# Optimization experiments

Hardware: AMD Instinct MI355X
Metric: run time of the kernel (lower is better)

Reference implementation:

```python
import jax, jax.numpy as jnp
import numpy as np

B, T, D_IN, H, D_OUT = 64, 512, 512, 1024, 512

def _uniform(key, shape, bound):
    return jax.random.uniform(key, shape, jnp.float32, -bound, bound)

def setup_inputs() -> dict:
    key = jax.random.key(0)
    ks = jax.random.split(key, 12)
    bnd = 1.0 / np.sqrt(H)  # PyTorch nn.RNN / nn.Linear init bound
    return {
        "x": jax.random.normal(ks[0], (B, T, D_IN), jnp.float32),
        "W_ih0": _uniform(ks[1], (H, D_IN), bnd),
        "W_hh0": _uniform(ks[2], (H, H), bnd),
        "b_ih0": _uniform(ks[3], (H,), bnd),
        "b_hh0": _uniform(ks[4], (H,), bnd),
        "W_ih1": _uniform(ks[5], (H, H), bnd),
        "W_hh1": _uniform(ks[6], (H, H), bnd),
        "b_ih1": _uniform(ks[7], (H,), bnd),
        "b_hh1": _uniform(ks[8], (H,), bnd),
        "W_fc": _uniform(ks[9], (D_OUT, H), bnd),
        "b_fc": _uniform(ks[10], (D_OUT,), bnd),
    }

def _rnn_layer(seq, W_ih, W_hh, b_ih, b_hh):
    # seq: [B, T, D]; tanh vanilla RNN, h0 = 0 (as in the torch forward)
    pre = jnp.einsum('btd,hd->bth', seq, W_ih) + b_ih  # input GEMM batched over time
    h0 = jnp.zeros((seq.shape[0], W_hh.shape[0]), seq.dtype)
    def step(h, p):
        h = jnp.tanh(p + h @ W_hh.T + b_hh)
        return h, h
    _, hs = jax.lax.scan(step, h0, jnp.swapaxes(pre, 0, 1))  # [T, B, H]
    return jnp.swapaxes(hs, 0, 1)  # [B, T, H]

def reference(x, W_ih0, W_hh0, b_ih0, b_hh0, W_ih1, W_hh1, b_ih1, b_hh1, W_fc, b_fc):
    h1 = _rnn_layer(x, W_ih0, W_hh0, b_ih0, b_hh0)
    h2 = _rnn_layer(h1, W_ih1, W_hh1, b_ih1, b_hh1)
    last = h2[:, -1, :]  # only the final timestep feeds the head
    return last @ W_fc.T + b_fc
```

## Files before the change

### kernel.cpp

```cpp
#include <hip/hip_runtime.h>
#include <stdint.h>

#define BB   64
#define TT   512
#define DIN  512
#define HH   1024
#define DOUT 512

#define GROUPS        4
#define ROWS          16
#define WGS_PER_GROUP 16
#define NSLICE        64
#define THREADS       512
#define NW            8
#define PSTR          18
#define PBUF          (NW * 4 * 16 * PSTR)
#define SENT          0x7fff7fffu

typedef __attribute__((ext_vector_type(8))) short frag8;
typedef __attribute__((ext_vector_type(4))) float f32x4;
typedef __attribute__((ext_vector_type(4))) unsigned int u32x4;

union U4F8 { u32x4 u; frag8 f; };

__device__ __forceinline__ float bf2f(unsigned short u) {
  union { unsigned int i; float f; } v; v.i = ((unsigned int)u) << 16; return v.f;
}
__device__ __forceinline__ unsigned short f2bf(float f) {
  union { float f; unsigned int i; } v; v.f = f;
  unsigned int x = v.i;
  x += 0x7fffu + ((x >> 16) & 1u);
  return (unsigned short)(x >> 16);
}
__device__ __forceinline__ frag8 ld8f32(const float* p) {
  frag8 r;
#pragma unroll
  for (int j = 0; j < 8; ++j) r[j] = (short)f2bf(p[j]);
  return r;
}

__device__ __forceinline__ bool ldx4_poll(frag8 a[4], const unsigned short* p) {
  u32x4 t0, t1, t2, t3;
  asm volatile(
      "global_load_dwordx4 %0, %4, off sc1\n\t"
      "global_load_dwordx4 %1, %4, off offset:64 sc1\n\t"
      "global_load_dwordx4 %2, %4, off offset:128 sc1\n\t"
      "global_load_dwordx4 %3, %4, off offset:192 sc1\n\t"
      "s_waitcnt vmcnt(0)"
      : "=&v"(t0), "=&v"(t1), "=&v"(t2), "=&v"(t3)
      : "v"(p)
      : "memory");
  bool ok = (t0[0] != SENT) & (t0[1] != SENT) & (t0[2] != SENT) & (t0[3] != SENT)
          & (t1[0] != SENT) & (t1[1] != SENT) & (t1[2] != SENT) & (t1[3] != SENT)
          & (t2[0] != SENT) & (t2[1] != SENT) & (t2[2] != SENT) & (t2[3] != SENT)
          & (t3[0] != SENT) & (t3[1] != SENT) & (t3[2] != SENT) & (t3[3] != SENT);
  U4F8 u;
  u.u = t0; a[0] = u.f;  u.u = t1; a[1] = u.f;
  u.u = t2; a[2] = u.f;  u.u = t3; a[3] = u.f;
  return __ballot(ok) == ~0ull;
}
__device__ __forceinline__ void st32_sc1(unsigned int* p, unsigned int v) {
  asm volatile("global_store_dword %0, %1, off sc1" :: "v"(p), "v"(v) : "memory");
}

template<int KIN, bool L0>
__device__ void scan_body(const void* Xv,
                          const float* Wih, const float* Whh,
                          const float* bih, const float* bhh,
                          unsigned short* S,
                          int g, int s, float* parts)
{
  constexpr int KIT_IN = KIN / (NW * 32);
  constexpr int KIT_HH = HH  / (NW * 32);

  const int j0  = s * NSLICE;
  const int r0  = g * ROWS;
  const int tid = threadIdx.x;
  const int w   = tid >> 6;
  const int l   = tid & 63;
  const int lm  = l & 15;
  const int lq  = l >> 4;

  frag8 wih_f[KIT_IN][4];
  frag8 whh_f[KIT_HH][4];
#pragma unroll
  for (int kit = 0; kit < KIT_IN; ++kit)
#pragma unroll
    for (int nt = 0; nt < 4; ++nt) {
      int n = j0 + nt * 16 + lm;
      int k = w * (KIN / NW) + kit * 32 + lq * 8;
      wih_f[kit][nt] = ld8f32(Wih + (size_t)n * KIN + k);
    }
#pragma unroll
  for (int kit = 0; kit < KIT_HH; ++kit)
#pragma unroll
    for (int nt = 0; nt < 4; ++nt) {
      int n = j0 + nt * 16 + lm;
      int k = w * (HH / NW) + kit * 32 + lq * 8;
      whh_f[kit][nt] = ld8f32(Whh + (size_t)n * HH + k);
    }

  const int erow = tid & 15;
  const int ecg  = tid >> 4;
  float bias2[2];
#pragma unroll
  for (int j = 0; j < 2; ++j) {
    int c = j0 + ecg * 2 + j;
    bias2[j] = bih[c] + bhh[c];
  }

  const size_t koff = (size_t)w * (KIN / NW) + (size_t)lq * 8;

  float4 xa[2 * KIT_IN];
  frag8  xf[KIT_IN];
  if constexpr (L0) {
    const float* xr = (const float*)Xv + ((size_t)(r0 + lm) * TT + 0) * KIN + koff;
#pragma unroll
    for (int kit = 0; kit < KIT_IN; ++kit) {
      xa[2 * kit]     = *(const float4*)(xr + kit * 32);
      xa[2 * kit + 1] = *(const float4*)(xr + kit * 32 + 4);
    }
  } else {
    const unsigned short* px = (const unsigned short*)Xv
        + ((size_t)(r0 + lm) * TT + 0) * KIN + koff;
    while (!ldx4_poll(xf, px)) {}
  }

  for (int t = 0; t < TT; ++t) {
    f32x4 acc[4];
#pragma unroll
    for (int nt = 0; nt < 4; ++nt) acc[nt] = (f32x4){0.f, 0.f, 0.f, 0.f};

    if constexpr (L0) {
#pragma unroll
      for (int kit = 0; kit < KIT_IN; ++kit) {
        const float* f0 = (const float*)&xa[2 * kit];
        const float* f1 = (const float*)&xa[2 * kit + 1];
        frag8 a;
#pragma unroll
        for (int j = 0; j < 4; ++j) {
          a[j]     = (short)f2bf(f0[j]);
          a[4 + j] = (short)f2bf(f1[j]);
        }
#pragma unroll
        for (int nt = 0; nt < 4; ++nt)
          acc[nt] = __builtin_amdgcn_mfma_f32_16x16x32_bf16(a, wih_f[kit][nt], acc[nt], 0, 0, 0);
      }
    } else {
#pragma unroll
      for (int kit = 0; kit < KIT_IN; ++kit)
#pragma unroll
        for (int nt = 0; nt < 4; ++nt)
          acc[nt] = __builtin_amdgcn_mfma_f32_16x16x32_bf16(xf[kit], wih_f[kit][nt], acc[nt], 0, 0, 0);
    }

    if (t > 0) {
      const unsigned short* ph = S + ((size_t)(r0 + lm) * TT + (t - 1)) * HH
                                   + (size_t)w * (HH / NW) + lq * 8;
      frag8 hf[KIT_HH];
      while (!ldx4_poll(hf, ph)) {}
      if constexpr (L0) {
        if (t + 1 < TT) {
          const float* xr = (const float*)Xv
              + ((size_t)(r0 + lm) * TT + (t + 1)) * KIN + koff;
#pragma unroll
          for (int kit = 0; kit < KIT_IN; ++kit) {
            xa[2 * kit]     = *(const float4*)(xr + kit * 32);
            xa[2 * kit + 1] = *(const float4*)(xr + kit * 32 + 4);
          }
        }
      }
#pragma unroll
      for (int kit = 0; kit < KIT_HH; ++kit)
#pragma unroll
        for (int nt = 0; nt < 4; ++nt)
          acc[nt] = __builtin_amdgcn_mfma_f32_16x16x32_bf16(hf[kit], whh_f[kit][nt], acc[nt], 0, 0, 0);
    } else if constexpr (L0) {
      const float* xr = (const float*)Xv + ((size_t)(r0 + lm) * TT + 1) * KIN + koff;
#pragma unroll
      for (int kit = 0; kit < KIT_IN; ++kit) {
        xa[2 * kit]     = *(const float4*)(xr + kit * 32);
        xa[2 * kit + 1] = *(const float4*)(xr + kit * 32 + 4);
      }
    }

    float* pb = parts + (t & 1) * PBUF;
#pragma unroll
    for (int nt = 0; nt < 4; ++nt)
#pragma unroll
      for (int r = 0; r < 4; ++r)
        pb[((w * 4 + nt) * 16 + lq * 4 + r) * PSTR + lm] = acc[nt][r];
    __syncthreads();

    unsigned int hb2 = 0;
#pragma unroll
    for (int j = 0; j < 2; ++j) {
      int c  = ecg * 2 + j;
      int nt = c >> 4;
      int lc = c & 15;
      float sm = 0.f;
#pragma unroll
      for (int w8 = 0; w8 < NW; ++w8)
        sm += pb[((w8 * 4 + nt) * 16 + erow) * PSTR + lc];
      float u = sm + bias2[j];
      float e = __expf(2.0f * u);
      float hv = 1.0f - 2.0f / (e + 1.0f);
      hb2 |= (unsigned int)f2bf(hv) << (16 * j);
    }
    unsigned short* dst = S + ((size_t)(r0 + erow) * TT + t) * HH + j0 + ecg * 2;
    st32_sc1((unsigned int*)dst, hb2);

    if constexpr (!L0) {
      if (t + 1 < TT) {
        const unsigned short* px = (const unsigned short*)Xv
            + ((size_t)(r0 + lm) * TT + (t + 1)) * KIN + koff;
        while (!ldx4_poll(xf, px)) {}
      }
    }
  }
}

__global__ __launch_bounds__(THREADS, 1)
void rnn_fused(const float* x,
               const float* Wih0, const float* Whh0, const float* bih0, const float* bhh0,
               const float* Wih1, const float* Whh1, const float* bih1, const float* bhh1,
               unsigned short* h1seq, unsigned short* h2seq)
{
  __shared__ float parts[2 * PBUF];
  const int wg = blockIdx.x;
  if (wg < GROUPS * WGS_PER_GROUP) {
    const int g = wg / WGS_PER_GROUP, s = wg % WGS_PER_GROUP;
    scan_body<DIN, true>(x, Wih0, Whh0, bih0, bhh0, h1seq, g, s, parts);
  } else {
    const int wg2 = wg - GROUPS * WGS_PER_GROUP;
    const int g = wg2 / WGS_PER_GROUP, s = wg2 % WGS_PER_GROUP;
    scan_body<HH, false>(h1seq, Wih1, Whh1, bih1, bhh1, h2seq, g, s, parts);
  }
}

__global__ void poison_kernel(uint4* __restrict__ p, int n4) {
  int i  = blockIdx.x * blockDim.x + threadIdx.x;
  int st = gridDim.x * blockDim.x;
  const uint4 v = make_uint4(SENT, SENT, SENT, SENT);
  for (; i < n4; i += st) p[i] = v;
}

__global__ void fc_kernel(const unsigned short* __restrict__ h2seq,
                          const float* __restrict__ Wfc,
                          const float* __restrict__ bfc,
                          float* __restrict__ out)
{
  int idx = blockIdx.x * blockDim.x + threadIdx.x;
  int m = idx >> 9;
  int n = idx & 511;
  const unsigned short* hp = h2seq + ((size_t)m * TT + (TT - 1)) * HH;
  const float*          wp = Wfc + (size_t)n * HH;
  float acc = 0.f;
#pragma unroll 4
  for (int k = 0; k < HH; k += 4) {
    ushort4 hv = *(const ushort4*)(hp + k);
    float4  wv = *(const float4*)(wp + k);
    acc += bf2f(hv.x) * wv.x + bf2f(hv.y) * wv.y
         + bf2f(hv.z) * wv.z + bf2f(hv.w) * wv.w;
  }
  out[idx] = acc + bfc[n];
}

extern "C" void kernel_launch(void* const* d_in, const int* in_sizes, int n_in,
                              void* d_out, int out_size, void* d_ws, size_t ws_size,
                              hipStream_t stream)
{
  const float* x    = (const float*)d_in[0];
  const float* Wih0 = (const float*)d_in[1];
  const float* Whh0 = (const float*)d_in[2];
  const float* bih0 = (const float*)d_in[3];
  const float* bhh0 = (const float*)d_in[4];
  const float* Wih1 = (const float*)d_in[5];
  const float* Whh1 = (const float*)d_in[6];
  const float* bih1 = (const float*)d_in[7];
  const float* bhh1 = (const float*)d_in[8];
  const float* Wfc  = (const float*)d_in[9];
  const float* bfc  = (const float*)d_in[10];

  unsigned char* ws = (unsigned char*)d_ws;
  unsigned short* h1seq = (unsigned short*)ws;
  unsigned short* h2seq = (unsigned short*)(ws + (size_t)BB * TT * HH * 2);

  poison_kernel<<<4096, 256, 0, stream>>>(
      (uint4*)ws, (int)(((size_t)BB * TT * HH * 2 * 2) / 16));

  rnn_fused<<<2 * GROUPS * WGS_PER_GROUP, THREADS, 0, stream>>>(
      x, Wih0, Whh0, bih0, bhh0, Wih1, Whh1, bih1, bhh1, h1seq, h2seq);

  fc_kernel<<<(BB * DOUT) / 256, 256, 0, stream>>>(h2seq, Wfc, bfc, (float*)d_out);
}
```

Before: 1.960 ms.

## Stage hidden-state stores through LDS, use wide stores and lighter polling

```diff
diff --git a/kernel.cpp b/kernel.cpp
--- a/kernel.cpp
+++ b/kernel.cpp
@@ -15,6 +15,7 @@
 #define NW            8
 #define PSTR          18
 #define PBUF          (NW * 4 * 16 * PSTR)
+#define SSTR          36
 #define SENT          0x7fff7fffu
 
 typedef __attribute__((ext_vector_type(8))) short frag8;
@@ -59,8 +60,28 @@
   u.u = t2; a[2] = u.f;  u.u = t3; a[3] = u.f;
   return __ballot(ok) == ~0ull;
 }
-__device__ __forceinline__ void st32_sc1(unsigned int* p, unsigned int v) {
-  asm volatile("global_store_dword %0, %1, off sc1" :: "v"(p), "v"(v) : "memory");
+__device__ __forceinline__ bool probe2(const unsigned short* p) {
+  u32x4 a, b;
+  asm volatile(
+      "global_load_dwordx4 %0, %2, off sc1\n\t"
+      "global_load_dwordx4 %1, %2, off offset:128 sc1\n\t"
+      "s_waitcnt vmcnt(0)"
+      : "=&v"(a), "=&v"(b)
+      : "v"(p)
+      : "memory");
+  bool ok = (a[0] != SENT) & (a[1] != SENT) & (a[2] != SENT) & (a[3] != SENT)
+          & (b[0] != SENT) & (b[1] != SENT) & (b[2] != SENT) & (b[3] != SENT);
+  return __ballot(ok) == ~0ull;
+}
+__device__ __forceinline__ void poll256(frag8 a[4], const unsigned short* p) {
+  if (ldx4_poll(a, p)) return;
+  for (;;) {
+    while (!probe2(p)) {}
+    if (ldx4_poll(a, p)) return;
+  }
+}
+__device__ __forceinline__ void st128_sc1(unsigned int* p, u32x4 v) {
+  asm volatile("global_store_dwordx4 %0, %1, off sc1" :: "v"(p), "v"(v) : "memory");
 }
 
 template<int KIN, bool L0>
@@ -68,7 +89,7 @@
                           const float* Wih, const float* Whh,
                           const float* bih, const float* bhh,
                           unsigned short* S,
-                          int g, int s, float* parts)
+                          int g, int s, float* parts, unsigned int* stage)
 {
   constexpr int KIT_IN = KIN / (NW * 32);
   constexpr int KIT_HH = HH  / (NW * 32);
@@ -108,6 +129,8 @@
     int c = j0 + ecg * 2 + j;
     bias2[j] = bih[c] + bhh[c];
   }
+  const int prow = tid >> 3;
+  const int pc8  = tid & 7;
 
   const size_t koff = (size_t)w * (KIN / NW) + (size_t)lq * 8;
 
@@ -123,7 +146,7 @@
   } else {
     const unsigned short* px = (const unsigned short*)Xv
         + ((size_t)(r0 + lm) * TT + 0) * KIN + koff;
-    while (!ldx4_poll(xf, px)) {}
+    poll256(xf, px);
   }
 
   for (int t = 0; t < TT; ++t) {
@@ -146,6 +169,15 @@
         for (int nt = 0; nt < 4; ++nt)
           acc[nt] = __builtin_amdgcn_mfma_f32_16x16x32_bf16(a, wih_f[kit][nt], acc[nt], 0, 0, 0);
       }
+      if (t + 1 < TT) {
+        const float* xr = (const float*)Xv
+            + ((size_t)(r0 + lm) * TT + (t + 1)) * KIN + koff;
+#pragma unroll
+        for (int kit = 0; kit < KIT_IN; ++kit) {
+          xa[2 * kit]     = *(const float4*)(xr + kit * 32);
+          xa[2 * kit + 1] = *(const float4*)(xr + kit * 32 + 4);
+        }
+      }
     } else {
 #pragma unroll
       for (int kit = 0; kit < KIT_IN; ++kit)
@@ -158,30 +190,12 @@
       const unsigned short* ph = S + ((size_t)(r0 + lm) * TT + (t - 1)) * HH
                                    + (size_t)w * (HH / NW) + lq * 8;
       frag8 hf[KIT_HH];
-      while (!ldx4_poll(hf, ph)) {}
-      if constexpr (L0) {
-        if (t + 1 < TT) {
-          const float* xr = (const float*)Xv
-              + ((size_t)(r0 + lm) * TT + (t + 1)) * KIN + koff;
-#pragma unroll
-          for (int kit = 0; kit < KIT_IN; ++kit) {
-            xa[2 * kit]     = *(const float4*)(xr + kit * 32);
-            xa[2 * kit + 1] = *(const float4*)(xr + kit * 32 + 4);
-          }
-        }
-      }
+      poll256(hf, ph);
 #pragma unroll
       for (int kit = 0; kit < KIT_HH; ++kit)
 #pragma unroll
         for (int nt = 0; nt < 4; ++nt)
           acc[nt] = __builtin_amdgcn_mfma_f32_16x16x32_bf16(hf[kit], whh_f[kit][nt], acc[nt], 0, 0, 0);
-    } else if constexpr (L0) {
-      const float* xr = (const float*)Xv + ((size_t)(r0 + lm) * TT + 1) * KIN + koff;
-#pragma unroll
-      for (int kit = 0; kit < KIT_IN; ++kit) {
-        xa[2 * kit]     = *(const float4*)(xr + kit * 32);
-        xa[2 * kit + 1] = *(const float4*)(xr + kit * 32 + 4);
-      }
     }
 
     float* pb = parts + (t & 1) * PBUF;
@@ -207,14 +221,20 @@
       float hv = 1.0f - 2.0f / (e + 1.0f);
       hb2 |= (unsigned int)f2bf(hv) << (16 * j);
     }
-    unsigned short* dst = S + ((size_t)(r0 + erow) * TT + t) * HH + j0 + ecg * 2;
-    st32_sc1((unsigned int*)dst, hb2);
+    stage[erow * SSTR + ecg] = hb2;
+    __syncthreads();
+
+    if (tid < 128) {
+      u32x4 v = *(const u32x4*)(stage + prow * SSTR + pc8 * 4);
+      unsigned short* dst = S + ((size_t)(r0 + prow) * TT + t) * HH + j0 + pc8 * 8;
+      st128_sc1((unsigned int*)dst, v);
+    }
 
     if constexpr (!L0) {
       if (t + 1 < TT) {
         const unsigned short* px = (const unsigned short*)Xv
             + ((size_t)(r0 + lm) * TT + (t + 1)) * KIN + koff;
-        while (!ldx4_poll(xf, px)) {}
+        poll256(xf, px);
       }
     }
   }
@@ -227,14 +247,15 @@
                unsigned short* h1seq, unsigned short* h2seq)
 {
   __shared__ float parts[2 * PBUF];
+  __shared__ unsigned int stage[16 * SSTR];
   const int wg = blockIdx.x;
   if (wg < GROUPS * WGS_PER_GROUP) {
     const int g = wg / WGS_PER_GROUP, s = wg % WGS_PER_GROUP;
-    scan_body<DIN, true>(x, Wih0, Whh0, bih0, bhh0, h1seq, g, s, parts);
+    scan_body<DIN, true>(x, Wih0, Whh0, bih0, bhh0, h1seq, g, s, parts, stage);
   } else {
     const int wg2 = wg - GROUPS * WGS_PER_GROUP;
     const int g = wg2 / WGS_PER_GROUP, s = wg2 % WGS_PER_GROUP;
-    scan_body<HH, false>(h1seq, Wih1, Whh1, bih1, bhh1, h2seq, g, s, parts);
+    scan_body<HH, false>(h1seq, Wih1, Whh1, bih1, bhh1, h2seq, g, s, parts, stage);
   }
 }
 
```

Result: faster. 1.859 ms (-5.2%).
